# Performance work log

Measured on AMD Instinct MI355X. Metric: run time of the kernel, lower is better.

## Reference

```python
import jax, jax.numpy as jnp
import numpy as np

THRESHOLD = 0.5
MARGIN = 0.5
MIN_PIXELS = 64


def make_grid(h, w):
    # Faithful to SpatialClustering.make_grid
    if w >= h:
        xm = jnp.broadcast_to(jnp.linspace(0.0, w / h, w).reshape(1, 1, w), (1, h, w))
        ym = jnp.broadcast_to(jnp.linspace(0.0, 1.0, h).reshape(1, h, 1), (1, h, w))
    else:
        xm = jnp.broadcast_to(jnp.linspace(0.0, 1.0, w).reshape(1, 1, w), (1, h, w))
        ym = jnp.broadcast_to(jnp.linspace(0.0, h / w, h).reshape(1, h, 1), (1, h, w))
    return jnp.concatenate([xm, ym], axis=0)  # (2, h, w)


def cluster_per_image(x, grid_flat):
    # x: (5, h, w); grid_flat: (2, N)
    c, h, w = x.shape
    N = h * w
    offset = x[0:2].reshape(2, N)
    sigma = x[2:4].reshape(2, N)
    seed_raw = x[4].reshape(N)

    spa_emb = jnp.tanh(offset) + grid_flat          # (2, N)
    seed_map = jax.nn.sigmoid(seed_raw)             # (N,)
    valid = seed_raw > THRESHOLD                    # (N,) == torch `mask`

    # In torch: masked_select restricts to `valid` pixels; here we keep the
    # full N-length arrays and carry `valid`/`unclustered` boolean masks.
    # unclustered starts as `valid`, so the torch outer guard
    # (mask.sum() > min_pixels) coincides with the first while-cond check.

    def cond(state):
        unclustered, inst, count, done = state
        return (jnp.sum(unclustered) > MIN_PIXELS) & jnp.logical_not(done)

    def body(state):
        unclustered, inst, count, done = state
        score = jnp.where(unclustered, seed_map, 0.0)
        idx = jnp.argmax(score)
        sc = score[idx]
        new_done = sc < THRESHOLD  # torch `break` -> revert this iteration's updates

        uncl2 = unclustered.at[idx].set(False)  # torch: unclustered[seed] = 0 before ratio
        center = spa_emb[:, idx]                # (2,)
        s = sigma[:, idx]                       # (2,)
        # exp(-sum((e-c)^2 / (2 s^2)))
        dist = jnp.exp(-jnp.sum((spa_emb - center[:, None]) ** 2 / (2.0 * s[:, None] ** 2), axis=0))  # (N,)
        proposal = (dist > MARGIN) & valid

        pc = jnp.sum(proposal)
        uc = jnp.sum(proposal & uncl2)
        # torch: proposal.sum() > min_pixels  and  unclustered[proposal].sum()/proposal.sum() > 0.5
        accept = (pc > MIN_PIXELS) & (2 * uc > pc)

        inst_new = jnp.where(accept & proposal, count, inst)
        count_new = count + accept.astype(jnp.int32)
        uncl_new = uncl2 & jnp.logical_not(proposal)  # torch: unclustered[proposal] = 0

        unclustered = jnp.where(new_done, unclustered, uncl_new)
        inst = jnp.where(new_done, inst, inst_new)
        count = jnp.where(new_done, count, count_new)
        return (unclustered, inst, count, new_done)

    init = (valid, jnp.zeros(N, dtype=jnp.int32), jnp.int32(1), jnp.array(False))
    _, inst, _, _ = jax.lax.while_loop(cond, body, init)
    return inst.reshape(h, w)


def setup_inputs() -> dict:
    key = jax.random.key(0)
    k1, k2, k3 = jax.random.split(key, 3)
    B, H, W = 4, 512, 1024
    offset = jax.random.normal(k1, (B, 2, H, W), dtype=jnp.float32)
    # sigma in [0.2, 0.45]: realistic per-pixel bandwidths so exp-distance
    # proposals cover cluster-sized regions and the greedy loop terminates.
    sigma = jax.random.uniform(k2, (B, 2, H, W), dtype=jnp.float32, minval=0.2, maxval=0.45)
    seed = jax.random.normal(k3, (B, 1, H, W), dtype=jnp.float32)
    tag_pred = jnp.concatenate([offset, sigma, seed], axis=1)  # (B, 5, H, W)
    return {"tag_pred": tag_pred}


def reference(tag_pred):
    b, c, h, w = tag_pred.shape
    grid_flat = make_grid(h, w).reshape(2, h * w)
    f = lambda x: cluster_per_image(x, grid_flat)
    inst = jax.lax.map(f, tag_pred)  # sequential per-image greedy clustering
    return inst.astype(jnp.uint8)    # (b, h, w) instance map, ids 0 = background
```

## Files before the change

### kernel.cpp

```cpp
#include <hip/hip_runtime.h>
#include <math.h>

#define BATCH 4
#define HH 512
#define WW 1024
#define NPIX (HH*WW)
#define CCAP 196608
#define GX 64
#define GY 48
#define NCELL (GX*GY)
#define CELL 0.0625f
#define INVCELL 16.0f
#define SEGSZ 512
#define NSEGMAX (CCAP/SEGSZ)
#define DLCAP 2048
#define CKCAP 800
#define CKBCAP 512

__device__ __forceinline__ float xla_tanhf(float x) {
  if (fabsf(x) < 0.0004f) return x;
  float xc = fminf(fmaxf(x, -7.90531110763549805f), 7.90531110763549805f);
  float x2 = __fmul_rn(xc, xc);
  float p = -2.76076847742355e-16f;
  p = fmaf(x2, p, 2.00018790482477e-13f);
  p = fmaf(x2, p, -8.60467152213735e-11f);
  p = fmaf(x2, p, 5.12229709037114e-08f);
  p = fmaf(x2, p, 1.48572235717979e-05f);
  p = fmaf(x2, p, 6.37261928875436e-04f);
  p = fmaf(x2, p, 4.89352455891786e-03f);
  p = __fmul_rn(xc, p);
  float q = fmaf(x2, 1.19825839466702e-06f, 1.18534705686654e-04f);
  q = fmaf(x2, q, 2.26843463243900e-03f);
  q = fmaf(x2, q, 4.89352518554385e-03f);
  return __fdiv_rn(p, q);
}

__device__ __forceinline__ float xla_expf(float x) {
  float xc = fminf(fmaxf(x, -87.3365478515625f), 88.72283935546875f);
  float m = floorf(fmaf(xc, 1.44269504088896341f, 0.5f));
  float r = fmaf(m, -0.693359375f, xc);
  r = fmaf(m, 2.12194440e-4f, r);
  float r2 = __fmul_rn(r, r);
  float p = 1.9875691500e-4f;
  p = fmaf(p, r, 1.3981999507e-3f);
  p = fmaf(p, r, 8.3334519073e-3f);
  p = fmaf(p, r, 4.1665795894e-2f);
  p = fmaf(p, r, 1.6666665459e-1f);
  p = fmaf(p, r, 5.0000001201e-1f);
  float y = fmaf(r2, p, r);
  y = __fadd_rn(y, 1.0f);
  return ldexpf(y, (int)m);
}

__device__ __forceinline__ float xla_sigmoidf(float x) {
  return fmaf(0.5f, xla_tanhf(__fmul_rn(0.5f, x)), 0.5f);
}

__device__ __forceinline__ bool prop_test(float2 e, float cx, float cy,
                                          float den0, float den1,
                                          float inv0, float inv1) {
  float d0 = __fsub_rn(e.x, cx), d1 = __fsub_rn(e.y, cy);
  float dd0 = __fmul_rn(d0, d0), dd1 = __fmul_rn(d1, d1);
  float zf = fmaf(dd0, inv0, __fmul_rn(dd1, inv1));
  if (zf < 0.6921472f) return true;
  if (zf <= 0.6941472f) {
    float t0 = __fdiv_rn(dd0, den0);
    float t1 = __fdiv_rn(dd1, den1);
    float z = __fadd_rn(t0, t1);
    return xla_expf(-z) > 0.5f;
  }
  return false;
}

__device__ __forceinline__ int cell_of_x(float ex) {
  int c = (int)((ex + 1.0f) * INVCELL);
  return min(max(c, 0), GX - 1);
}
__device__ __forceinline__ int cell_of_y(float ey) {
  int c = (int)((ey + 1.0f) * INVCELL);
  return min(max(c, 0), GY - 1);
}

__device__ __forceinline__ unsigned long long maskrange64(int a, int b) {
  unsigned long long mb = (b >= 64) ? ~0ULL : ((1ULL << b) - 1ULL);
  unsigned long long ma = (1ULL << a) - 1ULL;
  return mb & ~ma;
}

__device__ __forceinline__ unsigned wave_max_bcast_u32(unsigned x) {
  unsigned t;
  t = (unsigned)__builtin_amdgcn_update_dpp(0, (int)x, 0x111, 0xf, 0xf, false); if (t > x) x = t;
  t = (unsigned)__builtin_amdgcn_update_dpp(0, (int)x, 0x112, 0xf, 0xf, false); if (t > x) x = t;
  t = (unsigned)__builtin_amdgcn_update_dpp(0, (int)x, 0x114, 0xf, 0xf, false); if (t > x) x = t;
  t = (unsigned)__builtin_amdgcn_update_dpp(0, (int)x, 0x118, 0xf, 0xf, false); if (t > x) x = t;
  t = (unsigned)__builtin_amdgcn_update_dpp(0, (int)x, 0x142, 0xa, 0xf, false); if (t > x) x = t;
  t = (unsigned)__builtin_amdgcn_update_dpp(0, (int)x, 0x143, 0xc, 0xf, false); if (t > x) x = t;
  return (unsigned)__builtin_amdgcn_readlane((int)x, 63);
}

__device__ __forceinline__ int wave_sum_bcast_i32(int x) {
  x += __builtin_amdgcn_update_dpp(0, x, 0x111, 0xf, 0xf, false);
  x += __builtin_amdgcn_update_dpp(0, x, 0x112, 0xf, 0xf, false);
  x += __builtin_amdgcn_update_dpp(0, x, 0x114, 0xf, 0xf, false);
  x += __builtin_amdgcn_update_dpp(0, x, 0x118, 0xf, 0xf, false);
  x += __builtin_amdgcn_update_dpp(0, x, 0x142, 0xa, 0xf, false);
  x += __builtin_amdgcn_update_dpp(0, x, 0x143, 0xc, 0xf, false);
  return __builtin_amdgcn_readlane(x, 63);
}

__device__ __forceinline__ int wave_scan_incl_i32(int x) {
  x += __builtin_amdgcn_update_dpp(0, x, 0x111, 0xf, 0xf, false);
  x += __builtin_amdgcn_update_dpp(0, x, 0x112, 0xf, 0xf, false);
  x += __builtin_amdgcn_update_dpp(0, x, 0x114, 0xf, 0xf, false);
  x += __builtin_amdgcn_update_dpp(0, x, 0x118, 0xf, 0xf, false);
  x += __builtin_amdgcn_update_dpp(0, x, 0x142, 0xa, 0xf, false);
  x += __builtin_amdgcn_update_dpp(0, x, 0x143, 0xc, 0xf, false);
  return x;
}


__global__ __launch_bounds__(1024) void fill_kernel(int* out, int val, int n) {
  int i = blockIdx.x * 1024 + threadIdx.x;
  if (i < n) out[i] = val;
}

__global__ __launch_bounds__(1024) void hist_kernel(const float* __restrict__ in,
                                                    int* __restrict__ out,
                                                    int* __restrict__ hist) {
  __shared__ int lh[NCELL];
  int tid = threadIdx.x;
  int gid = blockIdx.x * 1024 + tid;
  int b = gid >> 19;
  int p = gid & (NPIX - 1);
  for (int j = tid; j < NCELL; j += 1024) lh[j] = 0;
  __syncthreads();
  const float* base = in + (size_t)b * 5 * NPIX;
  float seed = base[(size_t)4 * NPIX + p];
  out[gid] = 0;
  if (seed > 0.5f) {
    float ox = base[p];
    float oy = base[(size_t)NPIX + p];
    int col = p & (WW - 1);
    int row = p >> 10;
    float gx = __fmul_rn((float)col, 2.0f / 1023.0f);
    float gy = __fmul_rn((float)row, 1.0f / 511.0f);
    float ex = __fadd_rn(xla_tanhf(ox), gx);
    float ey = __fadd_rn(xla_tanhf(oy), gy);
    atomicAdd(&lh[cell_of_y(ey) * GX + cell_of_x(ex)], 1);
  }
  __syncthreads();
  for (int j = tid; j < NCELL; j += 1024) {
    int c = lh[j];
    if (c) atomicAdd(&hist[b * NCELL + j], c);
  }
}

__global__ __launch_bounds__(1024) void scan_kernel(const int* __restrict__ hist,
                                                    int* __restrict__ off,
                                                    int* __restrict__ cursor) {
  __shared__ int s_c[NCELL];
  __shared__ int s_ps[1024];
  int b = blockIdx.x, t = threadIdx.x;
  const int* h = hist + b * NCELL;
  for (int i = t; i < NCELL; i += 1024) s_c[i] = h[i];
  __syncthreads();
  int a = s_c[3 * t], b2 = s_c[3 * t + 1], c2 = s_c[3 * t + 2];
  int th = a + b2 + c2;
  s_ps[t] = th;
  __syncthreads();
  for (int d = 1; d < 1024; d <<= 1) {
    int v = (t >= d) ? s_ps[t - d] : 0;
    __syncthreads();
    s_ps[t] += v;
    __syncthreads();
  }
  int excl = s_ps[t] - th;
  int* ob = off + b * (NCELL + 1);
  int* cb = cursor + b * NCELL;
  ob[3 * t] = excl;              cb[3 * t] = excl;
  ob[3 * t + 1] = excl + a;      cb[3 * t + 1] = excl + a;
  ob[3 * t + 2] = excl + a + b2; cb[3 * t + 2] = excl + a + b2;
  if (t == 1023) ob[NCELL] = s_ps[1023];
}

__global__ __launch_bounds__(1024) void scatter_kernel(const float* __restrict__ in,
                                                       int* __restrict__ cursor,
                                                       float2* __restrict__ emb,
                                                       int2* __restrict__ pk) {
  __shared__ int lh[NCELL];
  __shared__ int lbase[NCELL];
  int tid = threadIdx.x;
  int gid = blockIdx.x * 1024 + tid;
  int b = gid >> 19;
  int p = gid & (NPIX - 1);
  for (int j = tid; j < NCELL; j += 1024) lh[j] = 0;
  __syncthreads();
  const float* base = in + (size_t)b * 5 * NPIX;
  float seed = base[(size_t)4 * NPIX + p];
  bool valid = seed > 0.5f;
  float ex = 0.0f, ey = 0.0f, smv = 0.0f;
  int cell = 0, sl = 0;
  if (valid) {
    float ox = base[p];
    float oy = base[(size_t)NPIX + p];
    int col = p & (WW - 1);
    int row = p >> 10;
    float gx = __fmul_rn((float)col, 2.0f / 1023.0f);
    float gy = __fmul_rn((float)row, 1.0f / 511.0f);
    ex = __fadd_rn(xla_tanhf(ox), gx);
    ey = __fadd_rn(xla_tanhf(oy), gy);
    smv = xla_sigmoidf(seed);
    cell = cell_of_y(ey) * GX + cell_of_x(ex);
    sl = atomicAdd(&lh[cell], 1);
  }
  __syncthreads();
  for (int j = tid; j < NCELL; j += 1024) {
    int c = lh[j];
    if (c) lbase[j] = atomicAdd(&cursor[b * NCELL + j], c);
  }
  __syncthreads();
  if (valid) {
    int slot = lbase[cell] + sl;
    if (slot < CCAP) {
      emb[(size_t)b * CCAP + slot] = make_float2(ex, ey);
      pk[(size_t)b * CCAP + slot]  = make_int2(__float_as_int(smv), p);
    }
  }
}

__device__ __forceinline__ void seg_rescan(int s, int V, int lane,
    const unsigned* s_uncl, const int2* __restrict__ pk,
    const float2* __restrict__ emb, const float* __restrict__ base,
    unsigned long long* s_segkey, int* s_segci, float4* s_segaux,
    float4* s_segaux2, bool checkAlive) {
  unsigned long long bk = 0ULL; int bci = -1; int bpx = 0;
  #pragma unroll
  for (int j = 0; j < 8; ++j) {
    int i = (s << 9) + (j << 6) + lane;
    if (i < V) {
      bool alive = !checkAlive || ((s_uncl[i >> 5] >> (i & 31)) & 1u);
      if (alive) {
        int2 v = pk[i];
        unsigned long long k = ((unsigned long long)(unsigned)v.x << 32) | (unsigned)(~v.y);
        if (k > bk) { bk = k; bci = i; bpx = v.y; }
      }
    }
  }
  unsigned bs = (unsigned)(bk >> 32);
  unsigned ms = wave_max_bcast_u32(bs);
  if (ms == 0u) {
    if (lane == 0) { s_segkey[s] = 0ULL; s_segci[s] = -1; }
    return;
  }
  unsigned long long tie = __ballot(bs == ms);
  bool winner;
  if (__popcll(tie) == 1ULL) {
    winner = (bs == ms);
  } else {
    unsigned long long mk = bk;
    #pragma unroll
    for (int o = 1; o < 64; o <<= 1) {
      unsigned long long ok = __shfl_xor(mk, o);
      if (ok > mk) mk = ok;
    }
    winner = (bk == mk);
  }
  if (winner) {
    s_segkey[s] = bk; s_segci[s] = bci;
    float2 e = emb[bci];
    float sxv = base[(size_t)2 * NPIX + bpx];
    float syv = base[(size_t)3 * NPIX + bpx];
    float d0 = __fmul_rn(2.0f, __fmul_rn(sxv, sxv));
    float d1 = __fmul_rn(2.0f, __fmul_rn(syv, syv));
    s_segaux[s] = make_float4(e.x, e.y, d0, d1);
    float i0v = 1.0f / d0;
    float i1v = 1.0f / d1;
    float ryv = sqrtf(__fmul_rn(d1, 0.6971472f)) * 1.00001f;
    s_segaux2[s] = make_float4(i0v, i1v, ryv, 0.0f);
  }
}

__global__ __launch_bounds__(1024) void cluster_kernel(const float* __restrict__ in,
                                                       int* __restrict__ out,
                                                       const float2* __restrict__ emb_all,
                                                       const int2* __restrict__ pk_all,
                                                       const int* __restrict__ off_g) {
  __shared__ unsigned int s_uncl[CCAP / 32];
  __shared__ int s_off[NCELL + 1];
  __shared__ unsigned long long s_segkey[NSEGMAX];
  __shared__ int s_segci[NSEGMAX];
  __shared__ float4 s_segaux[NSEGMAX];
  __shared__ float4 s_segaux2[NSEGMAX];
  __shared__ int s_dlist[DLCAP];
  __shared__ unsigned long long s_ck[CKCAP];
  __shared__ ulonglong2 s_ckbA[CKBCAP];
  __shared__ ulonglong2 s_ckbB[CKBCAP];
  __shared__ int s_pc[2];
  __shared__ int s_uc[2];
  __shared__ int s_nd[2];

  int b = blockIdx.x;
  int tid = threadIdx.x;
  int lane = tid & 63;
  int wid = tid >> 6;
  const int* offb = off_g + b * (NCELL + 1);
  int V = offb[NCELL];
  const float2* emb = emb_all + (size_t)b * CCAP;
  const int2*   pk  = pk_all  + (size_t)b * CCAP;
  int* outb = out + (size_t)b * NPIX;
  const float* base = in + (size_t)b * 5 * NPIX;

  if (V > CCAP) {
    for (int i = tid; i < NPIX; i += 1024) outb[i] = 1000000;
    return;
  }
  int NSEG = (V + SEGSZ - 1) >> 9;
  int Vm1 = V - 1;

  for (int i = tid; i <= NCELL; i += 1024) s_off[i] = offb[i];
  for (int w = tid; w < CCAP / 32; w += 1024) {
    int basebit = w << 5;
    unsigned m;
    if (basebit + 32 <= V)      m = 0xffffffffu;
    else if (basebit >= V)      m = 0u;
    else                        m = (1u << (V - basebit)) - 1u;
    s_uncl[w] = m;
  }
  if (tid < 2) { s_pc[tid] = 0; s_uc[tid] = 0; s_nd[tid] = 0; }
  __syncthreads();

  for (int s = wid; s < NSEG; s += 16)
    seg_rescan(s, V, lane, s_uncl, pk, emb, base, s_segkey, s_segci, s_segaux,
               s_segaux2, false);
  __syncthreads();

  int ucount = V, count = 1, guard = 0;
  int t = 0;
  while (ucount > 64 && guard++ <= CCAP) {
    int cur = t & 1, nxt = cur ^ 1;

    unsigned long long lk = 0ULL; int lsg = -1;
    for (int s = lane; s < NSEG; s += 64) {
      unsigned long long v = s_segkey[s];
      if (v > lk) { lk = v; lsg = s; }
    }
    unsigned ls = (unsigned)(lk >> 32);
    unsigned gs = wave_max_bcast_u32(ls);
    if (gs == 0u) break;
    float sm = __uint_as_float(gs);
    if (sm < 0.5f) break;
    unsigned long long bmask = __ballot(ls == gs);
    int src, sg;
    if (__popcll(bmask) == 1ULL) {
      src = __builtin_ctzll(bmask);
      sg = __shfl(lsg, src);
    } else {
      unsigned long long gk = lk;
      #pragma unroll
      for (int o = 1; o < 64; o <<= 1) {
        unsigned long long ok = __shfl_xor(gk, o);
        if (ok > gk) gk = ok;
      }
      unsigned long long bm2 = __ballot(lk == gk);
      src = __builtin_ctzll(bm2);
      sg = __shfl(lsg, src);
    }

    float4 aux = s_segaux[sg];
    float4 ax2 = s_segaux2[sg];
    float cx = aux.x, cy = aux.y, den0 = aux.z, den1 = aux.w;
    float inv0 = ax2.x;
    float inv1 = ax2.y;
    float ry = ax2.z;
    int r0 = cell_of_y(cy - ry);
    int r1 = cell_of_y(cy + ry);
    int nr = r1 - r0 + 1;

    int ck = 0, rs_l = 0, re_l = 0, m0_l = 0, m1_l = 0, startl = 0;
    if (lane < nr) {
      int r = r0 + lane;
      float ylo = fmaf((float)r, CELL, -1.0f);
      float dy = fmaxf(0.0f, fmaxf(ylo - cy, cy - (ylo + CELL))) * 0.999999f;
      float rem = 0.6971472f - dy * dy * inv1;
      if (rem > 0.0f) {
        float dxm = sqrtf(den0 * rem) * 1.00001f;
        int c0 = cell_of_x(cx - dxm), c1 = cell_of_x(cx + dxm);
        int rbase = r * GX;
        rs_l = s_off[rbase + c0]; re_l = s_off[rbase + c1 + 1];
        m0_l = rs_l; m1_l = rs_l;
        float dyc = fmaxf(fabsf(ylo - cy), fabsf(ylo + CELL - cy)) + 1e-5f;
        float remI = 0.6920f - dyc * dyc * inv1;
        if (remI > 0.0f) {
          float dxin = sqrtf(den0 * remI) * 0.9999f;
          int a  = (int)ceilf(fmaf(cx - dxin, INVCELL, INVCELL) + 1e-3f);
          int bb = (int)floorf(fmaf(cx + dxin, INVCELL, INVCELL) - 1e-3f) - 1;
          a = max(a, c0); bb = min(bb, c1);
          if (a <= bb) { m0_l = s_off[rbase + a]; m1_l = s_off[rbase + bb + 1]; }
        }
        startl = rs_l & ~31;
        ck = (re_l > rs_l) ? ((re_l - startl + 255) >> 8) : 0;
      }
    }
    int cum = wave_scan_incl_i32(ck);
    int nc = __builtin_amdgcn_readlane(cum, 63);
    int excl = cum - ck;
    if (lane < nr && ck) {
      for (int k = 0; k < ck; ++k) {
        int i0k = startl + (k << 8);
        int ssk = max(rs_l - i0k, 0);
        int lok = min(max(m0_l - i0k, 0), 256);
        int h2k = min(max(m1_l - i0k, 0), 256);
        int enk = min(re_l - i0k, 256);
        s_ck[excl + k] = (unsigned long long)(unsigned)(i0k >> 5)
                       | ((unsigned long long)(unsigned)ssk << 13)
                       | ((unsigned long long)(unsigned)lok << 19)
                       | ((unsigned long long)(unsigned)h2k << 28)
                       | ((unsigned long long)(unsigned)enk << 37);
      }
    }

    int pc = 0, uc = 0;
    int c = wid;
    unsigned long long ed = (c < nc) ? s_ck[c] : 0ULL;
    while (c < nc) {
      int cn = c + 16;
      unsigned long long epre = (cn < nc) ? s_ck[cn] : 0ULL;
      int i0 = ((int)(ed & 0x1fff)) << 5;
      int ss = (int)((ed >> 13) & 0x3f);
      int lo = (int)((ed >> 19) & 0x1ff);
      int h2 = (int)((ed >> 28) & 0x1ff);
      int en = (int)((ed >> 37) & 0x1ff);
      bool interior = (lo <= ss && h2 >= en);
      unsigned long long bm0, bm1, bm2, bm3;
      if (interior) {
        bm0 = maskrange64(ss, min(en, 64));
        bm1 = maskrange64(0, min(max(en - 64, 0), 64));
        bm2 = maskrange64(0, min(max(en - 128, 0), 64));
        bm3 = maskrange64(0, min(max(en - 192, 0), 64));
      } else {
        int idx1 = lane + 64, idx2 = lane + 128, idx3 = lane + 192;
        int ia = min(i0 + lane, Vm1),  ib = min(i0 + idx1, Vm1);
        int ic = min(i0 + idx2, Vm1),  id = min(i0 + idx3, Vm1);
        float2 e0 = emb[ia], e1 = emb[ib], e2 = emb[ic], e3 = emb[id];
        bool t0 = prop_test(e0, cx, cy, den0, den1, inv0, inv1);
        bool t1 = prop_test(e1, cx, cy, den0, den1, inv0, inv1);
        bool t2 = prop_test(e2, cx, cy, den0, den1, inv0, inv1);
        bool t3 = prop_test(e3, cx, cy, den0, den1, inv0, inv1);
        bool p0 = (lane >= ss && lane < en) && ((lane >= lo && lane < h2) || t0);
        bool p1 = (idx1 < en) && ((idx1 >= lo && idx1 < h2) || t1);
        bool p2 = (idx2 < en) && ((idx2 >= lo && idx2 < h2) || t2);
        bool p3 = (idx3 < en) && ((idx3 >= lo && idx3 < h2) || t3);
        bm0 = __ballot(p0);
        bm1 = __ballot(p1);
        bm2 = __ballot(p2);
        bm3 = __ballot(p3);
        if (c < CKBCAP) {
          if (lane == 0)      { ulonglong2 v; v.x = bm0; v.y = bm1; s_ckbA[c] = v; }
          else if (lane == 1) { ulonglong2 v; v.x = bm2; v.y = bm3; s_ckbB[c] = v; }
        }
      }
      if ((bm0 | bm1 | bm2 | bm3) != 0ULL && lane < 8) {
        unsigned long long bsel = (lane < 2) ? bm0 : (lane < 4) ? bm1
                                 : (lane < 6) ? bm2 : bm3;
        unsigned bits = (unsigned)(bsel >> ((lane & 1) << 5));
        pc += __popc(bits);
        if (bits) {
          unsigned tw = (unsigned)(i0 >> 5) + (unsigned)lane;
          unsigned old = atomicAnd(&s_uncl[tw], ~bits);
          unsigned remv = old & bits;
          if (remv) {
            uc += __popc(remv);
            int seg = (int)(tw >> 4);
            int ciw = s_segci[seg];
            if ((ciw >> 5) == (int)tw && ((remv >> (ciw & 31)) & 1u)) {
              int pos = atomicAdd(&s_nd[cur], 1);
              if (pos < DLCAP) s_dlist[pos] = seg;
            }
          }
        }
      }
      c = cn; ed = epre;
    }
    int pcW = wave_sum_bcast_i32(pc);
    int ucW = wave_sum_bcast_i32(uc);
    if (lane == 0 && (pcW | ucW)) {
      if (pcW) atomicAdd(&s_pc[cur], pcW);
      if (ucW) atomicAdd(&s_uc[cur], ucW);
    }
    __syncthreads();

    int pcT = s_pc[cur];
    int ucR = s_uc[cur];
    int ndRaw = s_nd[cur];
    bool accept = (pcT > 64) && (2 * (ucR - 1) > pcT);
    int label = count & 255;
    if (accept) count++;
    ucount -= ucR;
    if (tid == 0) { s_pc[nxt] = 0; s_uc[nxt] = 0; s_nd[nxt] = 0; }

    if (accept) {
      for (int c2 = wid; c2 < nc; c2 += 16) {
        unsigned long long e = s_ck[c2];
        int i0 = ((int)(e & 0x1fff)) << 5;
        int ss = (int)((e >> 13) & 0x3f);
        int lo = (int)((e >> 19) & 0x1ff);
        int h2 = (int)((e >> 28) & 0x1ff);
        int en = (int)((e >> 37) & 0x1ff);
        bool interior = (lo <= ss && h2 >= en);
        if (interior) {
          unsigned long long b0 = maskrange64(ss, min(en, 64));
          unsigned long long b1 = maskrange64(0, min(max(en - 64, 0), 64));
          unsigned long long b2 = maskrange64(0, min(max(en - 128, 0), 64));
          unsigned long long b3 = maskrange64(0, min(max(en - 192, 0), 64));
          if ((b0 >> lane) & 1ULL) outb[pk[i0 + lane].y] = label;
          if ((b1 >> lane) & 1ULL) outb[pk[i0 + 64 + lane].y] = label;
          if ((b2 >> lane) & 1ULL) outb[pk[i0 + 128 + lane].y] = label;
          if ((b3 >> lane) & 1ULL) outb[pk[i0 + 192 + lane].y] = label;
        } else if (c2 < CKBCAP) {
          ulonglong2 ba = s_ckbA[c2];
          ulonglong2 bb = s_ckbB[c2];
          if ((ba.x >> lane) & 1ULL) outb[pk[i0 + lane].y] = label;
          if ((ba.y >> lane) & 1ULL) outb[pk[i0 + 64 + lane].y] = label;
          if ((bb.x >> lane) & 1ULL) outb[pk[i0 + 128 + lane].y] = label;
          if ((bb.y >> lane) & 1ULL) outb[pk[i0 + 192 + lane].y] = label;
        } else {
          #pragma unroll
          for (int g = 0; g < 4; ++g) {
            int idx = (g << 6) + lane;
            if (idx >= ss && idx < en &&
                ((idx >= lo && idx < h2) ||
                 prop_test(emb[i0 + idx], cx, cy, den0, den1, inv0, inv1)))
              outb[pk[i0 + idx].y] = label;
          }
        }
      }
    }

    if (ndRaw > DLCAP) {
      for (int s = wid; s < NSEG; s += 16)
        seg_rescan(s, V, lane, s_uncl, pk, emb, base, s_segkey, s_segci,
                   s_segaux, s_segaux2, true);
    } else {
      for (int d = wid; d < ndRaw; d += 16)
        seg_rescan(s_dlist[d], V, lane, s_uncl, pk, emb, base, s_segkey,
                   s_segci, s_segaux, s_segaux2, true);
    }
    __syncthreads();
    t++;
  }
}


extern "C" void kernel_launch(void* const* d_in, const int* in_sizes, int n_in,
                              void* d_out, int out_size, void* d_ws, size_t ws_size,
                              hipStream_t stream) {
  const float* in = (const float*)d_in[0];
  int* out = (int*)d_out;

  size_t hist_bytes = (size_t)BATCH * NCELL * sizeof(int);
  size_t off_bytes  = (size_t)BATCH * (NCELL + 1) * sizeof(int);
  size_t cur_bytes  = (size_t)BATCH * NCELL * sizeof(int);
  size_t emb_bytes  = (size_t)BATCH * CCAP * sizeof(float2);
  size_t pk_bytes   = (size_t)BATCH * CCAP * sizeof(int2);

  size_t o_hist = 256;
  size_t o_off  = (o_hist + hist_bytes + 255) & ~(size_t)255;
  size_t o_cur  = (o_off + off_bytes + 255) & ~(size_t)255;
  size_t o_emb  = (o_cur + cur_bytes + 255) & ~(size_t)255;
  size_t o_pk   = (o_emb + emb_bytes + 255) & ~(size_t)255;
  size_t need   = o_pk + pk_bytes;

  if (ws_size < need) {
    fill_kernel<<<(out_size + 1023) / 1024, 1024, 0, stream>>>(out, 2000000, out_size);
    return;
  }

  int*    hist = (int*)((char*)d_ws + o_hist);
  int*    off  = (int*)((char*)d_ws + o_off);
  int*    cur  = (int*)((char*)d_ws + o_cur);
  float2* emb  = (float2*)((char*)d_ws + o_emb);
  int2*   pk   = (int2*)((char*)d_ws + o_pk);

  hipMemsetAsync(hist, 0, hist_bytes, stream);
  hist_kernel<<<(BATCH * NPIX) / 1024, 1024, 0, stream>>>(in, out, hist);
  scan_kernel<<<BATCH, 1024, 0, stream>>>(hist, off, cur);
  scatter_kernel<<<(BATCH * NPIX) / 1024, 1024, 0, stream>>>(in, cur, emb, pk);
  cluster_kernel<<<BATCH, 1024, 0, stream>>>(in, out, emb, pk, off);
}
```

Measured before the change: 793.4 us.

## Overlap next-seed segment argmax with proposal pass and validate after rescan

Computes a speculative argmax over segment keys, excluding the current seed's segment, before the block-wide barrier. This overlaps the argmax with other waves' proposal work. After the dirty-segment rescan, it checks whether that candidate's key is unchanged and compares it with the current segment's refreshed key, falling back to a full argmax only if the candidate was modified. This removes the serial per-iteration argmax from the critical path but adds a speculative scan that may be wasted, plus extra validation logic. Correctness relies on keys only ever decreasing or staying the same during rescans.

```diff
diff --git a/kernel.cpp b/kernel.cpp
--- a/kernel.cpp
+++ b/kernel.cpp
@@ -116,6 +116,37 @@
   x += __builtin_amdgcn_update_dpp(0, x, 0x142, 0xa, 0xf, false);
   x += __builtin_amdgcn_update_dpp(0, x, 0x143, 0xc, 0xf, false);
   return x;
+}
+
+__device__ __forceinline__ void seg_argmax(const unsigned long long* s_segkey,
+                                           int NSEG, int lane, int skip,
+                                           int &outSg, unsigned long long &outKey) {
+  unsigned long long lk = 0ULL; int lsg = -1;
+  for (int s = lane; s < NSEG; s += 64) {
+    if (s == skip) continue;
+    unsigned long long v = s_segkey[s];
+    if (v > lk) { lk = v; lsg = s; }
+  }
+  unsigned ls = (unsigned)(lk >> 32);
+  unsigned gs = wave_max_bcast_u32(ls);
+  if (gs == 0u) { outSg = -1; outKey = 0ULL; return; }
+  unsigned long long bmask = __ballot(ls == gs);
+  if (__popcll(bmask) == 1ULL) {
+    int src = __builtin_ctzll(bmask);
+    outSg = __shfl(lsg, src);
+    outKey = __shfl(lk, src);
+  } else {
+    unsigned long long gk = lk;
+    #pragma unroll
+    for (int o = 1; o < 64; o <<= 1) {
+      unsigned long long ok = __shfl_xor(gk, o);
+      if (ok > gk) gk = ok;
+    }
+    unsigned long long bm2 = __ballot(lk == gk);
+    int src = __builtin_ctzll(bm2);
+    outSg = __shfl(lsg, src);
+    outKey = gk;
+  }
 }
 
 
@@ -336,35 +367,12 @@
 
   int ucount = V, count = 1, guard = 0;
   int t = 0;
+  int sg; unsigned long long sgKey;
+  seg_argmax(s_segkey, NSEG, lane, -1, sg, sgKey);
   while (ucount > 64 && guard++ <= CCAP) {
+    if (sg < 0) break;
+    if (__uint_as_float((unsigned)(sgKey >> 32)) < 0.5f) break;
     int cur = t & 1, nxt = cur ^ 1;
-
-    unsigned long long lk = 0ULL; int lsg = -1;
-    for (int s = lane; s < NSEG; s += 64) {
-      unsigned long long v = s_segkey[s];
-      if (v > lk) { lk = v; lsg = s; }
-    }
-    unsigned ls = (unsigned)(lk >> 32);
-    unsigned gs = wave_max_bcast_u32(ls);
-    if (gs == 0u) break;
-    float sm = __uint_as_float(gs);
-    if (sm < 0.5f) break;
-    unsigned long long bmask = __ballot(ls == gs);
-    int src, sg;
-    if (__popcll(bmask) == 1ULL) {
-      src = __builtin_ctzll(bmask);
-      sg = __shfl(lsg, src);
-    } else {
-      unsigned long long gk = lk;
-      #pragma unroll
-      for (int o = 1; o < 64; o <<= 1) {
-        unsigned long long ok = __shfl_xor(gk, o);
-        if (ok > gk) gk = ok;
-      }
-      unsigned long long bm2 = __ballot(lk == gk);
-      src = __builtin_ctzll(bm2);
-      sg = __shfl(lsg, src);
-    }
 
     float4 aux = s_segaux[sg];
     float4 ax2 = s_segaux2[sg];
@@ -481,6 +489,10 @@
       }
       c = cn; ed = epre;
     }
+
+    int staleArg; unsigned long long staleKey;
+    seg_argmax(s_segkey, NSEG, lane, sg, staleArg, staleKey);
+
     int pcW = wave_sum_bcast_i32(pc);
     int ucW = wave_sum_bcast_i32(uc);
     if (lane == 0 && (pcW | ucW)) {
@@ -546,6 +558,19 @@
                    s_segci, s_segaux, s_segaux2, true);
     }
     __syncthreads();
+
+    unsigned long long kOwn = s_segkey[sg];
+    if (staleArg >= 0) {
+      unsigned long long kStale = s_segkey[staleArg];
+      if (kStale == staleKey) {
+        if (kOwn > staleKey) { sgKey = kOwn; }
+        else { sg = staleArg; sgKey = staleKey; }
+      } else {
+        seg_argmax(s_segkey, NSEG, lane, -1, sg, sgKey);
+      }
+    } else {
+      if (kOwn != 0ULL) { sgKey = kOwn; } else { sg = -1; }
+    }
     t++;
   }
 }
```

Measured after the change: 822.9 us. +3.7%, slower.
